# Performance work log

Measured on AMD Instinct MI355X. Metric: run time of the kernel, lower is better.

The kernel has to match this reference:

```python
import jax, jax.numpy as jnp
import numpy as np

PI = 3.141592657  # constant used verbatim in the original module


def _shift(a, dy, dx):
    # out[i, j] = a[i + dy, j + dx], zero-padded at the border (matches conv2d padding=1)
    h, w = a.shape
    p = jnp.pad(a, 1)
    return jax.lax.dynamic_slice(p, (1 + dy, 1 + dx), (h, w))


def setup_inputs() -> dict:
    key = jax.random.key(0)
    h, w = 2048, 4096
    # realistic metric depth in [1, 80] meters
    depth = jax.random.uniform(key, (h, w), dtype=jnp.float32, minval=1.0, maxval=80.0)
    fx = fy = 1000.0
    cx, cy = w / 2.0, h / 2.0
    cam_param = jnp.array([[fx, 0.0, cx], [0.0, fy, cy], [0.0, 0.0, 1.0]], dtype=jnp.float32)
    return {"depth": depth, "cam_param": cam_param, "sign_filter": 1}


def _nim_forward(depth, cam_param, sign_filter):
    h, w = depth.shape
    fx = cam_param[0, 0]
    fy = cam_param[1, 1]
    cx = cam_param[0, 2]
    cy = cam_param[1, 2]

    v = jnp.arange(h, dtype=jnp.float32)[:, None]
    u = jnp.arange(w, dtype=jnp.float32)[None, :]

    Z = depth
    Y = Z * (v - cy) / fx  # original uses camParam[0,0] for Y as well
    X = Z * (u - cx) / fx
    neg = Y <= 0
    Z = jnp.where(neg, 0.0, Z)
    Y = jnp.where(neg, 0.0, Y)
    Z = jnp.where(jnp.isnan(Z), 0.0, Z)

    D = 1.0 / Z  # disparity-like map; inf where Z == 0, as in torch

    # Gx = [[0,0,0],[-1,0,1],[0,0,0]], Gy = [[0,-1,0],[0,0,0],[0,1,0]] (cross-correlation)
    Gu = _shift(D, 0, 1) - _shift(D, 0, -1)
    Gv = _shift(D, 1, 0) - _shift(D, -1, 0)
    nx_t = Gu * fx
    ny_t = Gv * fy

    phi = jnp.arctan(ny_t / nx_t) + PI
    a = jnp.cos(phi)
    b = jnp.sin(phi)

    # the 4 diff kernels compute X[i,j] - X[i+dy, j+dx] for these neighbor offsets
    dirs = ((-1, 0), (0, -1), (0, 1), (1, 0))

    def diffs(A):
        return jnp.stack([A - _shift(A, dy, dx) for dy, dx in dirs])  # (4, h, w)

    X_d, Y_d, Z_d = diffs(X), diffs(Y), diffs(Z)

    nz_i = -(nx_t[None] * X_d + ny_t[None] * Y_d) / Z_d  # (4, h, w)
    norm = jnp.sqrt(nx_t[None] ** 2 + ny_t[None] ** 2 + nz_i ** 2)
    nxv = nx_t[None] / norm
    nyv = ny_t[None] / norm
    nzv = nz_i / norm
    nxv = jnp.where(jnp.isnan(nxv), 0.0, nxv)
    nyv = jnp.where(jnp.isnan(nyv), 0.0, nyv)
    nzv = jnp.where(jnp.isnan(nzv), 0.0, nzv)

    if sign_filter:
        n_pos = jnp.sum(nzv > 0, axis=0, keepdims=True)
        n_neg = jnp.sum(nzv < 0, axis=0, keepdims=True)
        pos_mask = (n_pos >= n_neg) & (nzv > 0)
        neg_mask = (n_pos < n_neg) & (nzv < 0)
        fm = (pos_mask | neg_mask).astype(jnp.float32)
        nxv = nxv * fm
        nyv = nyv * fm
        nzv = nzv * fm

    theta = jnp.arctan((jnp.sum(nxv, 0) * a + jnp.sum(nyv, 0) * b) / jnp.sum(nzv, 0))
    nx = jnp.sin(theta) * a
    ny = jnp.sin(theta) * b
    nz = jnp.cos(theta)
    bad = jnp.isnan(nz)
    nx = jnp.where(bad, 0.0, nx)
    ny = jnp.where(bad, 0.0, ny)
    nz = jnp.where(bad, -1.0, nz)

    sign_map = jnp.where(ny > 0, -1.0, 1.0)
    return jnp.stack([nx * sign_map, ny * sign_map, nz * sign_map])  # (3, h, w)


def reference(depth, cam_param, sign_filter):
    return _nim_forward(depth, cam_param, sign_filter)
```

## Files before the change

kernel.cpp:

```cpp
#include <hip/hip_runtime.h>
#include <math.h>

#define HH 2048
#define WW 4096

__device__ __forceinline__ float rcp_f(float x){ return __builtin_amdgcn_rcpf(x); }
__device__ __forceinline__ float rsq_f(float x){ return __builtin_amdgcn_rsqf(x); }

__global__ __launch_bounds__(256)
void nim_kernel(const float* __restrict__ depth,
                const float* __restrict__ cam,
                const int*   __restrict__ signf,
                float* __restrict__ out)
{
    const int j0 = (blockIdx.x * 256 + threadIdx.x) * 4;
    const int i  = blockIdx.y;
    const size_t HW  = (size_t)HH * WW;
    const size_t idx = (size_t)i * WW + j0;

    const float cy = cam[5];

    float4* o0 = (float4*)(out + idx);
    float4* o1 = (float4*)(out + HW + idx);
    float4* o2 = (float4*)(out + 2 * HW + idx);

    if ((float)i <= cy + 1.0f){
        *o0 = make_float4(0.f, 0.f, 0.f, 0.f);
        *o1 = make_float4(0.f, 0.f, 0.f, 0.f);
        *o2 = make_float4(-1.f, -1.f, -1.f, -1.f);
        return;
    }

    const float fx = cam[0], cx = cam[2], fy = cam[4];
    const float inv_fx = rcp_f(fx);
    const int   sf = signf[0];

    const float rf_u = ((float)(i - 1) - cy) * inv_fx;
    const float rf_c = ((float)i       - cy) * inv_fx;
    const float rf_d = ((float)(i + 1) - cy) * inv_fx;

    const float4 c4 = *(const float4*)(depth + (size_t)i * WW + j0);
    const float4 u4 = *(const float4*)(depth + (size_t)(i - 1) * WW + j0);
    float4 d4 = make_float4(0.f, 0.f, 0.f, 0.f);
    const bool dvalid = (i + 1 < HH);
    if (dvalid) d4 = *(const float4*)(depth + (size_t)(i + 1) * WW + j0);

    const bool lvalid = (j0 > 0);
    const bool rvalid = (j0 + 4 < WW);
    const float cl = lvalid ? depth[(size_t)i * WW + j0 - 1] : 0.f;
    const float cr = rvalid ? depth[(size_t)i * WW + j0 + 4] : 0.f;

    float cf[6];
#pragma unroll
    for (int t = 0; t < 6; ++t)
        cf[t] = ((float)(j0 - 1 + t) - cx) * inv_fx;

    float dc[6] = {cl, c4.x, c4.y, c4.z, c4.w, cr};
    float Xc[6], Yc[6], Zc[6], Dc[6];
#pragma unroll
    for (int t = 0; t < 6; ++t){
        Xc[t] = dc[t] * cf[t];
        Yc[t] = dc[t] * rf_c;
        Zc[t] = dc[t];
        Dc[t] = rcp_f(dc[t]);
    }
    if (!lvalid){ Xc[0]=0.f; Yc[0]=0.f; Zc[0]=0.f; Dc[0]=0.f; }
    if (!rvalid){ Xc[5]=0.f; Yc[5]=0.f; Zc[5]=0.f; Dc[5]=0.f; }

    const float du[4] = {u4.x, u4.y, u4.z, u4.w};
    const float dd[4] = {d4.x, d4.y, d4.z, d4.w};
    float Xu[4], Yu[4], Zu[4], Du[4], Xd4[4], Yd4[4], Zd4[4], Dd[4];
#pragma unroll
    for (int t = 0; t < 4; ++t){
        Xu[t]  = du[t] * cf[t + 1];
        Yu[t]  = du[t] * rf_u;
        Zu[t]  = du[t];
        Du[t]  = rcp_f(du[t]);
        Xd4[t] = dd[t] * cf[t + 1];
        Yd4[t] = dd[t] * rf_d;
        Zd4[t] = dd[t];
        Dd[t]  = rcp_f(dd[t]);
    }
    if (!dvalid){
#pragma unroll
        for (int t = 0; t < 4; ++t){ Xd4[t]=0.f; Yd4[t]=0.f; Zd4[t]=0.f; Dd[t]=0.f; }
    }

    float ox[4], oy[4], oz[4];
#pragma unroll
    for (int p = 0; p < 4; ++p){
        const float nx = (Dc[p + 2] - Dc[p]) * fx;
        const float ny = (Dd[p] - Du[p]) * fy;
        const float r2 = nx * nx + ny * ny;
        const float rr = rsq_f(r2);
        const float rs = copysignf(rr, nx);
        const float a = -nx * rs;
        const float b = -ny * rs;

        const float CX = Xc[p + 1], CY = Yc[p + 1], CZ = Zc[p + 1];
        const float NX[4] = {Xu[p], Xc[p], Xc[p + 2], Xd4[p]};
        const float NY[4] = {Yu[p], Yc[p], Yc[p + 2], Yd4[p]};
        const float NZ[4] = {Zu[p], Zc[p], Zc[p + 2], Zd4[p]};

        float vxs[4], vys[4], vzs[4];
        int npos = 0, nneg = 0;
#pragma unroll
        for (int k = 0; k < 4; ++k){
            const float Xd = CX - NX[k];
            const float Yd = CY - NY[k];
            const float w  = CZ - NZ[k];
            const float g  = nx * Xd + ny * Yd;
            const float arg = (r2 * w) * w + g * g;
            const float rn  = rsq_f(arg);
            const float h   = fabsf(w) * rn;
            float vx = nx * h;
            float vy = ny * h;
            float vz = -g * copysignf(rn, w);
            const bool za = (arg == 0.f);
            if (za){ vx = 0.f; vy = 0.f; }
            if (za || (w == 0.f)) vz = 0.f;
            vxs[k] = vx; vys[k] = vy; vzs[k] = vz;
            npos += (vz > 0.f);
            nneg += (vz < 0.f);
        }

        float sx = 0.f, sy = 0.f, sz = 0.f;
#pragma unroll
        for (int k = 0; k < 4; ++k){
            const float vz = vzs[k];
            const bool keep = !sf ||
                ((npos >= nneg) && (vz > 0.f)) ||
                ((npos <  nneg) && (vz < 0.f));
            const float fm = keep ? 1.f : 0.f;
            sx += vxs[k] * fm;
            sy += vys[k] * fm;
            sz += vzs[k] * fm;
        }

        const float q  = (sx * a + sy * b) * rcp_f(sz);
        const float q2 = q * q;
        const float ct = rsq_f(1.f + q2);
        float st = q * ct;
        if (isinf(q2)) st = copysignf(1.f, q);

        float onx = st * a, ony = st * b, onz = ct;
        if (isnan(onz)){ onx = 0.f; ony = 0.f; onz = -1.f; }
        const float sgn = (ony > 0.f) ? -1.f : 1.f;
        ox[p] = onx * sgn; oy[p] = ony * sgn; oz[p] = onz * sgn;
    }

    *o0 = make_float4(ox[0], ox[1], ox[2], ox[3]);
    *o1 = make_float4(oy[0], oy[1], oy[2], oy[3]);
    *o2 = make_float4(oz[0], oz[1], oz[2], oz[3]);
}

extern "C" void kernel_launch(void* const* d_in, const int* in_sizes, int n_in,
                              void* d_out, int out_size, void* d_ws, size_t ws_size,
                              hipStream_t stream) {
    const float* depth = (const float*)d_in[0];
    const float* cam   = (const float*)d_in[1];
    const int*   signf = (const int*)d_in[2];
    float* out = (float*)d_out;

    dim3 block(256, 1, 1);
    dim3 grid(WW / (256 * 4), HH, 1);
    nim_kernel<<<grid, block, 0, stream>>>(depth, cam, signf, out);
}
```

Measured before the change: 134.0 us.

## Process 8 pixels per thread, simplify normal math, use nontemporal stores

Each thread now handles 8 columns instead of 4, which halves the grid and amortizes the halo loads and per-thread setup. The inner normal computation is simplified algebraically: the x/y sums collapse into a single scalar H, because a and b are parallel to nx and ny. Neighbor X/Y differences are also computed directly from depth, with no precomputed arrays. All output writes become nontemporal vector stores to avoid polluting the cache. The changes raise register pressure and may reorder floating-point results slightly.

```diff
diff --git a/kernel.cpp b/kernel.cpp
--- a/kernel.cpp
+++ b/kernel.cpp
@@ -7,27 +7,33 @@
 __device__ __forceinline__ float rcp_f(float x){ return __builtin_amdgcn_rcpf(x); }
 __device__ __forceinline__ float rsq_f(float x){ return __builtin_amdgcn_rsqf(x); }
 
+typedef float vf4 __attribute__((ext_vector_type(4)));
+
+__device__ __forceinline__ void st_nt4(float* p, float a, float b, float c, float d){
+    vf4 v = {a, b, c, d};
+    __builtin_nontemporal_store(v, (vf4*)p);
+}
+
 __global__ __launch_bounds__(256)
 void nim_kernel(const float* __restrict__ depth,
                 const float* __restrict__ cam,
                 const int*   __restrict__ signf,
                 float* __restrict__ out)
 {
-    const int j0 = (blockIdx.x * 256 + threadIdx.x) * 4;
+    const int j0 = (blockIdx.x * 256 + threadIdx.x) * 8;
     const int i  = blockIdx.y;
     const size_t HW  = (size_t)HH * WW;
     const size_t idx = (size_t)i * WW + j0;
 
     const float cy = cam[5];
 
-    float4* o0 = (float4*)(out + idx);
-    float4* o1 = (float4*)(out + HW + idx);
-    float4* o2 = (float4*)(out + 2 * HW + idx);
-
     if ((float)i <= cy + 1.0f){
-        *o0 = make_float4(0.f, 0.f, 0.f, 0.f);
-        *o1 = make_float4(0.f, 0.f, 0.f, 0.f);
-        *o2 = make_float4(-1.f, -1.f, -1.f, -1.f);
+        st_nt4(out + idx,              0.f, 0.f, 0.f, 0.f);
+        st_nt4(out + idx + 4,          0.f, 0.f, 0.f, 0.f);
+        st_nt4(out + HW + idx,         0.f, 0.f, 0.f, 0.f);
+        st_nt4(out + HW + idx + 4,     0.f, 0.f, 0.f, 0.f);
+        st_nt4(out + 2*HW + idx,      -1.f,-1.f,-1.f,-1.f);
+        st_nt4(out + 2*HW + idx + 4,  -1.f,-1.f,-1.f,-1.f);
         return;
     }
 
@@ -39,105 +45,106 @@
     const float rf_c = ((float)i       - cy) * inv_fx;
     const float rf_d = ((float)(i + 1) - cy) * inv_fx;
 
-    const float4 c4 = *(const float4*)(depth + (size_t)i * WW + j0);
-    const float4 u4 = *(const float4*)(depth + (size_t)(i - 1) * WW + j0);
-    float4 d4 = make_float4(0.f, 0.f, 0.f, 0.f);
-    const bool dvalid = (i + 1 < HH);
-    if (dvalid) d4 = *(const float4*)(depth + (size_t)(i + 1) * WW + j0);
+    const float* rowc = depth + (size_t)i * WW + j0;
+    const float* rowu = depth + (size_t)(i - 1) * WW + j0;
 
-    const bool lvalid = (j0 > 0);
-    const bool rvalid = (j0 + 4 < WW);
-    const float cl = lvalid ? depth[(size_t)i * WW + j0 - 1] : 0.f;
-    const float cr = rvalid ? depth[(size_t)i * WW + j0 + 4] : 0.f;
+    float dc[10], du[8], dd[8];
+    {
+        const float4 a = *(const float4*)rowc;
+        const float4 b = *(const float4*)(rowc + 4);
+        dc[1]=a.x; dc[2]=a.y; dc[3]=a.z; dc[4]=a.w;
+        dc[5]=b.x; dc[6]=b.y; dc[7]=b.z; dc[8]=b.w;
+        const float4 ua = *(const float4*)rowu;
+        const float4 ub = *(const float4*)(rowu + 4);
+        du[0]=ua.x; du[1]=ua.y; du[2]=ua.z; du[3]=ua.w;
+        du[4]=ub.x; du[5]=ub.y; du[6]=ub.z; du[7]=ub.w;
+    }
+    const bool lv = (j0 > 0);
+    const bool rv = (j0 + 8 < WW);
+    dc[0] = lv ? rowc[-1] : 0.f;
+    dc[9] = rv ? rowc[8]  : 0.f;
 
-    float cf[6];
+    const bool dv = (i + 1 < HH);
+    if (dv){
+        const float* rowd = depth + (size_t)(i + 1) * WW + j0;
+        const float4 da = *(const float4*)rowd;
+        const float4 db = *(const float4*)(rowd + 4);
+        dd[0]=da.x; dd[1]=da.y; dd[2]=da.z; dd[3]=da.w;
+        dd[4]=db.x; dd[5]=db.y; dd[6]=db.z; dd[7]=db.w;
+    } else {
 #pragma unroll
-    for (int t = 0; t < 6; ++t)
-        cf[t] = ((float)(j0 - 1 + t) - cx) * inv_fx;
-
-    float dc[6] = {cl, c4.x, c4.y, c4.z, c4.w, cr};
-    float Xc[6], Yc[6], Zc[6], Dc[6];
-#pragma unroll
-    for (int t = 0; t < 6; ++t){
-        Xc[t] = dc[t] * cf[t];
-        Yc[t] = dc[t] * rf_c;
-        Zc[t] = dc[t];
-        Dc[t] = rcp_f(dc[t]);
-    }
-    if (!lvalid){ Xc[0]=0.f; Yc[0]=0.f; Zc[0]=0.f; Dc[0]=0.f; }
-    if (!rvalid){ Xc[5]=0.f; Yc[5]=0.f; Zc[5]=0.f; Dc[5]=0.f; }
-
-    const float du[4] = {u4.x, u4.y, u4.z, u4.w};
-    const float dd[4] = {d4.x, d4.y, d4.z, d4.w};
-    float Xu[4], Yu[4], Zu[4], Du[4], Xd4[4], Yd4[4], Zd4[4], Dd[4];
-#pragma unroll
-    for (int t = 0; t < 4; ++t){
-        Xu[t]  = du[t] * cf[t + 1];
-        Yu[t]  = du[t] * rf_u;
-        Zu[t]  = du[t];
-        Du[t]  = rcp_f(du[t]);
-        Xd4[t] = dd[t] * cf[t + 1];
-        Yd4[t] = dd[t] * rf_d;
-        Zd4[t] = dd[t];
-        Dd[t]  = rcp_f(dd[t]);
-    }
-    if (!dvalid){
-#pragma unroll
-        for (int t = 0; t < 4; ++t){ Xd4[t]=0.f; Yd4[t]=0.f; Zd4[t]=0.f; Dd[t]=0.f; }
+        for (int t = 0; t < 8; ++t) dd[t] = 0.f;
     }
 
-    float ox[4], oy[4], oz[4];
+    float Dc[10], Du[8], Dd[8];
 #pragma unroll
-    for (int p = 0; p < 4; ++p){
+    for (int t = 0; t < 10; ++t) Dc[t] = rcp_f(dc[t]);
+    if (!lv) Dc[0] = 0.f;
+    if (!rv) Dc[9] = 0.f;
+#pragma unroll
+    for (int t = 0; t < 8; ++t){
+        Du[t] = rcp_f(du[t]);
+        Dd[t] = dv ? rcp_f(dd[t]) : 0.f;
+    }
+
+    const float jb = ((float)(j0 - 1) - cx) * inv_fx;
+
+    float ox[8], oy[8], oz[8];
+#pragma unroll
+    for (int p = 0; p < 8; ++p){
+        const float cfl = jb + (float)p       * inv_fx;
+        const float cfc = jb + (float)(p + 1) * inv_fx;
+        const float cfr = jb + (float)(p + 2) * inv_fx;
+        const float CZ  = dc[p + 1];
+
         const float nx = (Dc[p + 2] - Dc[p]) * fx;
         const float ny = (Dd[p] - Du[p]) * fy;
         const float r2 = nx * nx + ny * ny;
         const float rr = rsq_f(r2);
         const float rs = copysignf(rr, nx);
-        const float a = -nx * rs;
-        const float b = -ny * rs;
+        const float a  = -nx * rs;
+        const float b  = -ny * rs;
 
-        const float CX = Xc[p + 1], CY = Yc[p + 1], CZ = Zc[p + 1];
-        const float NX[4] = {Xu[p], Xc[p], Xc[p + 2], Xd4[p]};
-        const float NY[4] = {Yu[p], Yc[p], Yc[p + 2], Yd4[p]};
-        const float NZ[4] = {Zu[p], Zc[p], Zc[p + 2], Zd4[p]};
-
-        float vxs[4], vys[4], vzs[4];
+        float hk[4], vzk[4];
         int npos = 0, nneg = 0;
 #pragma unroll
         for (int k = 0; k < 4; ++k){
-            const float Xd = CX - NX[k];
-            const float Yd = CY - NY[k];
-            const float w  = CZ - NZ[k];
-            const float g  = nx * Xd + ny * Yd;
+            float NZ, Xd, Yd;
+            if (k == 0){ NZ = du[p];     const float w0 = CZ - NZ;
+                         Xd = cfc * w0;  Yd = rf_c * CZ - rf_u * NZ; }
+            else if (k == 1){ NZ = dc[p];     Xd = cfc * CZ - cfl * NZ;
+                              Yd = rf_c * (CZ - NZ); }
+            else if (k == 2){ NZ = dc[p + 2]; Xd = cfc * CZ - cfr * NZ;
+                              Yd = rf_c * (CZ - NZ); }
+            else            { NZ = dd[p];     const float w0 = CZ - NZ;
+                              Xd = cfc * w0;  Yd = rf_c * CZ - rf_d * NZ; }
+            const float w   = CZ - NZ;
+            const float g   = nx * Xd + ny * Yd;
             const float arg = (r2 * w) * w + g * g;
             const float rn  = rsq_f(arg);
-            const float h   = fabsf(w) * rn;
-            float vx = nx * h;
-            float vy = ny * h;
+            float h  = fabsf(w) * rn;
             float vz = -g * copysignf(rn, w);
             const bool za = (arg == 0.f);
-            if (za){ vx = 0.f; vy = 0.f; }
+            if (za) h = 0.f;
             if (za || (w == 0.f)) vz = 0.f;
-            vxs[k] = vx; vys[k] = vy; vzs[k] = vz;
+            hk[k] = h; vzk[k] = vz;
             npos += (vz > 0.f);
             nneg += (vz < 0.f);
         }
 
-        float sx = 0.f, sy = 0.f, sz = 0.f;
+        const bool posm = (npos >= nneg);
+        float H = 0.f, sz = 0.f;
 #pragma unroll
         for (int k = 0; k < 4; ++k){
-            const float vz = vzs[k];
-            const bool keep = !sf ||
-                ((npos >= nneg) && (vz > 0.f)) ||
-                ((npos <  nneg) && (vz < 0.f));
+            const float vz = vzk[k];
+            const bool keep = !sf || (posm ? (vz > 0.f) : (vz < 0.f));
             const float fm = keep ? 1.f : 0.f;
-            sx += vxs[k] * fm;
-            sy += vys[k] * fm;
-            sz += vzs[k] * fm;
+            H  += hk[k] * fm;
+            sz += vz    * fm;
         }
 
-        const float q  = (sx * a + sy * b) * rcp_f(sz);
+        const float cs = copysignf(r2 * rr, nx);
+        const float q  = (-cs * H) * rcp_f(sz);
         const float q2 = q * q;
         const float ct = rsq_f(1.f + q2);
         float st = q * ct;
@@ -149,9 +156,12 @@
         ox[p] = onx * sgn; oy[p] = ony * sgn; oz[p] = onz * sgn;
     }
 
-    *o0 = make_float4(ox[0], ox[1], ox[2], ox[3]);
-    *o1 = make_float4(oy[0], oy[1], oy[2], oy[3]);
-    *o2 = make_float4(oz[0], oz[1], oz[2], oz[3]);
+    st_nt4(out + idx,            ox[0], ox[1], ox[2], ox[3]);
+    st_nt4(out + idx + 4,        ox[4], ox[5], ox[6], ox[7]);
+    st_nt4(out + HW + idx,       oy[0], oy[1], oy[2], oy[3]);
+    st_nt4(out + HW + idx + 4,   oy[4], oy[5], oy[6], oy[7]);
+    st_nt4(out + 2*HW + idx,     oz[0], oz[1], oz[2], oz[3]);
+    st_nt4(out + 2*HW + idx + 4, oz[4], oz[5], oz[6], oz[7]);
 }
 
 extern "C" void kernel_launch(void* const* d_in, const int* in_sizes, int n_in,
@@ -163,6 +173,6 @@
     float* out = (float*)d_out;
 
     dim3 block(256, 1, 1);
-    dim3 grid(WW / (256 * 4), HH, 1);
+    dim3 grid(WW / (256 * 8), HH, 1);
     nim_kernel<<<grid, block, 0, stream>>>(depth, cam, signf, out);
 }
```

After: 140.1 us. 4.6% more time.
